# Performance work log

Hardware: AMD Instinct MI355X
Metric: run time of the kernel (lower is better)

The kernel has to match this reference:

```python
import jax, jax.numpy as jnp
import numpy as np

# hyperparameters (init_kwargs)
T = 0.1
MARGIN = 0.0
NEG_IOU = 0.5
K = 2              # pos_topk
WEIGHT = 1.0
EXPONENT = 2.0
NEG_SAMPLES = 512  # neg_samples_num
START_DNS_EPOCH = 1

# static problem sizes
B, SPB, TPS = 16, 2, 4          # videos, sentences/video, targets/sentence
N, C = 64, 256                  # clips, channels
S = B * SPB                     # total sentences = 32
M = S * TPS                     # total moments = 128


def setup_inputs() -> dict:
    key = jax.random.key(0)
    k1, k2, k3, k4 = jax.random.split(key, 4)
    return {
        "video_feats": jax.random.normal(k1, (S, C, N, N), jnp.float32),
        "sents_feats": jax.random.normal(k2, (S, C), jnp.float32),
        "num_sentences": jnp.full((B,), SPB, jnp.int32),
        "num_targets": jnp.full((S,), TPS, jnp.int32),
        "iou2d": jax.random.uniform(k3, (S, N, N), jnp.float32),
        "iou2ds": jax.random.uniform(k4, (M, N, N), jnp.float32),
        "mask2d": jnp.triu(jnp.ones((N, N), bool)),  # 2D-TAN valid-proposal mask
        "epoch": 2,
    }


def _normalize(x):
    return x / jnp.maximum(jnp.linalg.norm(x, axis=-1, keepdims=True), 1e-12)


def _loss_core(video_feats, sents_feats, iou2d, iou2ds,
               num_sentences, num_targets, mask2d, epoch):
    S_, C_, N_, _ = video_feats.shape
    B_ = num_sentences.shape[0]
    M_ = iou2ds.shape[0]
    P = N_ * (N_ + 1) // 2  # number of True in upper-triangular mask2d

    # masked_select(mask2d) -> gather flat proposal positions (static size P)
    flat_idx = jnp.nonzero(mask2d.reshape(-1), size=P)[0]
    vf = video_feats.reshape(S_, C_, N_ * N_)[:, :, flat_idx]        # (S,C,P)
    vf = _normalize(vf.transpose(0, 2, 1))                            # (S,P,C)
    _ = _normalize(sents_feats)                                       # normalized but unused downstream
    iou2d_f = iou2d.reshape(S_, -1)[:, flat_idx]                      # (S,P)
    iou2ds_f = iou2ds.reshape(M_, -1)[:, flat_idx]                    # (M,P)

    scatter_m2s = jnp.repeat(jnp.arange(S_), num_targets, total_repeat_length=M_)
    scatter_s2b = jnp.repeat(jnp.arange(B_), num_sentences, total_repeat_length=S_)
    scatter_b2s = jnp.concatenate([jnp.zeros((1,), jnp.int32),
                                   jnp.cumsum(num_sentences)[:-1].astype(jnp.int32)])

    # all (ref, pos) pairs within each sentence's num_targets*K topk slots (uniform -> static)
    nK = (M_ // S_) * K
    base = (jnp.arange(S_) * nK)[:, None, None]
    i = jnp.arange(nK)
    zero = jnp.zeros((nK,), jnp.int32)
    ref_idx = (base + i[None, :, None] + zero[None, None, :]).reshape(-1)   # (E,)
    pos_idx = (base + zero[None, :, None] + i[None, None, :]).reshape(-1)   # (E,)
    scatter_e2s = jnp.repeat(jnp.arange(S_), nK * nK)                        # (E,)

    # top-K proposals per moment by IoU
    topk_idx = jax.lax.top_k(iou2ds_f, K)[1]                                 # (M,K)
    allm = vf[scatter_m2s]                                                   # (M,P,C)
    topk_vf = jnp.take_along_axis(allm, topk_idx[:, :, None], axis=1)        # (M,K,C)
    pos_vf = topk_vf.reshape(M_ * K, C_)

    intra_pos = jnp.sum(pos_vf[ref_idx] * pos_vf[pos_idx], axis=-1)          # (E,)
    bank = vf[scatter_b2s].reshape(B_ * P, C_)                               # one sentence per video
    intra_all = pos_vf @ bank.T                                              # (M*K, B*P)

    # positive mask: own-video block, refined by iou2d > neg_iou
    own = scatter_s2b[:, None] == jnp.arange(B_)[None, :]                    # (S,B)
    s2v_pos = iou2d_f > NEG_IOU                                              # (S,P)
    pos_mask = jnp.where(own[:, :, None], s2v_pos[:, None, :], False).reshape(S_, B_ * P)

    if epoch >= START_DNS_EPOCH:
        # DNS: similarity-weighted negative sampling without replacement (Gumbel top-k)
        sim = (jnp.einsum('mkc,pc->mkp', topk_vf, bank).mean(axis=1) + 1.0) * 0.5   # (M,B*P)
        fused = jax.ops.segment_sum(sim, scatter_m2s, num_segments=S_)
        fused = fused / num_targets[:, None].astype(sim.dtype)                      # per-sentence mean
        fused = jnp.where(pos_mask, 0.0, fused ** EXPONENT)                          # (S,B*P)
        logw = jnp.where(fused > 0, jnp.log(jnp.maximum(fused, 1e-30)), -jnp.inf)
        u = jax.random.uniform(jax.random.key(42), fused.shape, minval=1e-7, maxval=1.0 - 1e-7)
        gumbel = -jnp.log(-jnp.log(u))
        samp_idx = jax.lax.top_k(logw + gumbel, NEG_SAMPLES)[1]                      # (S,NEG_SAMPLES)
        neg_mask = jnp.zeros((S_, B_ * P), jnp.float32).at[
            jnp.arange(S_)[:, None], samp_idx].set(1.0)
    else:
        neg_mask = (~pos_mask).astype(jnp.float32)

    # LogCrossEntropy (InfoNCE with explicit negative mask)
    all_e = intra_all[ref_idx]            # (E, B*P)
    neg_e = neg_mask[scatter_e2s]         # (E, B*P)
    pos_logit = (intra_pos - MARGIN) / T
    neg_sum = jnp.sum(jnp.exp(all_e / T) * neg_e, axis=-1)
    loss = jnp.mean(-(pos_logit - jnp.log(jnp.exp(pos_logit) + neg_sum)))
    return loss


def reference(video_feats, sents_feats, num_sentences, num_targets,
              iou2d, iou2ds, mask2d, epoch):
    loss = _loss_core(video_feats, sents_feats, iou2d, iou2ds,
                      num_sentences, num_targets, mask2d, epoch)
    return (loss * WEIGHT, loss)
```

## Files before the change

kernel.cpp:

```cpp
#include <hip/hip_runtime.h>
#include <math.h>
#include <stdint.h>

#define S_    32
#define BV_   16
#define M_    128
#define C_    256
#define NN    4096
#define P_    2080
#define BP    33280
#define NSAMP 512
#define EQCAP 2048

__device__ __forceinline__ uint32_t rotl32(uint32_t x, int n){ return (x<<n) | (x>>(32-n)); }

__device__ __forceinline__ void threefry2x32(uint32_t k0, uint32_t k1, uint32_t &x0, uint32_t &x1){
  uint32_t ks2 = k0 ^ k1 ^ 0x1BD11BDAu;
  x0 += k0; x1 += k1;
  #define TF_R(r) { x0 += x1; x1 = rotl32(x1, r); x1 ^= x0; }
  TF_R(13) TF_R(15) TF_R(26) TF_R(6)
  x0 += k1;  x1 += ks2 + 1u;
  TF_R(17) TF_R(29) TF_R(16) TF_R(24)
  x0 += ks2; x1 += k0 + 2u;
  TF_R(13) TF_R(15) TF_R(26) TF_R(6)
  x0 += k0;  x1 += k1 + 3u;
  TF_R(17) TF_R(29) TF_R(16) TF_R(24)
  x0 += k1;  x1 += ks2 + 4u;
  TF_R(13) TF_R(15) TF_R(26) TF_R(6)
  x0 += ks2; x1 += k0 + 5u;
  #undef TF_R
}

__global__ __launch_bounds__(256) void k_prep(const float* __restrict__ iou2ds,
                                              const float* __restrict__ vfeat,
                                              float* __restrict__ pos_vf,
                                              float* __restrict__ qsumT,
                                              int* __restrict__ counter){
  const int s = blockIdx.x;
  const int t = threadIdx.x;
  __shared__ float sv1[256], sv2[256];
  __shared__ int   si1[256], si2[256];
  __shared__ int   fpk_s[8];
  __shared__ float wsum[4];
  __shared__ float s_inv;

  if(s==0 && t==0) *counter = 0;

  for(int q=0; q<4; ++q){
    const float* row = iou2ds + (size_t)(s*4 + q)*NN;
    float v1=-1e30f, v2=-1e30f; int i1=0x7FFFFFFF, i2=0x7FFFFFFF;
    for(int f=t; f<NN; f+=256){
      int ti = f>>6, tj = f&63;
      if(tj < ti) continue;
      float v = row[f];
      if(v > v1 || (v == v1 && f < i1)){ v2=v1; i2=i1; v1=v; i1=f; }
      else if(v > v2 || (v == v2 && f < i2)){ v2=v; i2=f; }
    }
    sv1[t]=v1; sv2[t]=v2; si1[t]=i1; si2[t]=i2;
    for(int stp=128; stp>0; stp>>=1){
      __syncthreads();
      if(t < stp){
        float a1=sv1[t], a2=sv2[t]; int x1=si1[t], x2=si2[t];
        float b1=sv1[t+stp], b2=sv2[t+stp]; int y1=si1[t+stp], y2=si2[t+stp];
        float m1v, m2v; int m1i, m2i;
        bool aTop = (a1 > b1) || (a1 == b1 && x1 < y1);
        if(aTop){
          m1v=a1; m1i=x1;
          if((a2 > b1) || (a2 == b1 && x2 < y1)){ m2v=a2; m2i=x2; } else { m2v=b1; m2i=y1; }
        } else {
          m1v=b1; m1i=y1;
          if((b2 > a1) || (b2 == a1 && y2 < x1)){ m2v=b2; m2i=y2; } else { m2v=a1; m2i=x1; }
        }
        sv1[t]=m1v; sv2[t]=m2v; si1[t]=m1i; si2[t]=m2i;
      }
    }
    __syncthreads();
    if(t==0){ fpk_s[q*2+0]=si1[0]; fpk_s[q*2+1]=si2[0]; }
    __syncthreads();
  }

  float v[8];
  #pragma unroll
  for(int r=0;r<8;r++) v[r] = vfeat[((size_t)s*C_ + t)*NN + fpk_s[r]];

  float qs = 0.f;
  for(int r=0; r<8; ++r){
    float ss = v[r]*v[r];
    for(int o=32;o>0;o>>=1) ss += __shfl_down(ss, o, 64);
    if((t&63)==0) wsum[t>>6]=ss;
    __syncthreads();
    if(t==0){
      float tot = wsum[0]+wsum[1]+wsum[2]+wsum[3];
      s_inv = 1.0f / fmaxf(sqrtf(tot), 1e-12f);
    }
    __syncthreads();
    float pv = v[r] * s_inv;
    pos_vf[(size_t)(s*8+r)*C_ + t] = pv;
    qs += pv;
  }
  qsumT[t*32 + s] = qs;
}

__global__ __launch_bounds__(256) void k_bankkeys(const float* __restrict__ vfeat,
                                                  const float* __restrict__ qsumT,
                                                  const float* __restrict__ iou2d,
                                                  float* __restrict__ bank,
                                                  unsigned int* __restrict__ ukey){
  extern __shared__ char dyn_sm[];
  float* tile = (float*)dyn_sm;
  float* ssp  = (float*)dyn_sm + 256*65;
  float* invs = (float*)dyn_sm + 256*65 + 256;

  const int i = blockIdx.x;
  const int b = blockIdx.y;
  const int t = threadIdx.x;
  const int j = t & 63, cq = t >> 6;
  const float* basep = vfeat + (size_t)(2*b)*C_*NN + (size_t)i*64;

  float ssq = 0.f;
  for(int it=0; it<64; ++it){
    int cc = it*4 + cq;
    float v = basep[(size_t)cc*NN + j];
    tile[cc*65 + j] = v;
    ssq += v*v;
  }
  ssp[t] = ssq;
  __syncthreads();
  if(t < 64){
    float tot = ssp[t]+ssp[64+t]+ssp[128+t]+ssp[192+t];
    invs[t] = 1.0f/fmaxf(sqrtf(tot), 1e-12f);
  }
  __syncthreads();

  const int start = 64*i - (i*(i-1))/2;
  for(int jj=i; jj<64; ++jj){
    size_t row = (size_t)b*P_ + start + (jj - i);
    bank[row*C_ + t] = tile[t*65 + jj] * invs[jj];
  }

  const int lane = t & 63;
  const int sbase = __builtin_amdgcn_readfirstlane((t >> 6) * 8);
  float acc[8];
  #pragma unroll
  for(int k=0;k<8;k++) acc[k]=0.f;
  #pragma unroll 4
  for(int cc=0; cc<256; ++cc){
    float v = tile[cc*65 + lane];
    const float* qc = qsumT + cc*32 + sbase;
    #pragma unroll
    for(int k=0;k<8;k++) acc[k] = fmaf(qc[k], v, acc[k]);
  }

  if(lane >= i){
    const int jg = b*P_ + start + (lane - i);
    const int fp = i*64 + lane;
    const float iou0 = iou2d[(size_t)(2*b)*NN + fp];
    const float iou1 = iou2d[(size_t)(2*b+1)*NN + fp];
    const float inv_j = invs[lane];
    #pragma unroll 1
    for(int k=0;k<8;k++){
      const int sIdx = sbase + k;
      float fz = 0.0625f*(acc[k]*inv_j) + 0.5f;
      bool pos = ((sIdx>>1)==b) && (((sIdx&1)?iou1:iou0) > 0.5f);
      float val = pos ? 0.f : fz*fz;
      float key;
      if(val > 0.f){
        float logw = logf(fmaxf(val, 1e-30f));
        unsigned int f = (unsigned int)(sIdx*BP + jg);
        const unsigned int HALF = 532480u;
        bool second = f >= HALF;
        uint32_t x0 = second ? (f - HALF) : f;
        uint32_t x1 = second ? f : (f + HALF);
        threefry2x32(0u, 42u, x0, x1);
        uint32_t bits = second ? x1 : x0;
        uint32_t fb = (bits >> 9) | 0x3f800000u;
        float f01 = __uint_as_float(fb) - 1.0f;
        const float mn = 1e-7f, mx = 1.0f - 1e-7f;
        float u = fmaxf(mn, f01*(mx-mn) + mn);
        float g = -logf(-logf(u));
        key = logw + g;
      } else {
        key = -INFINITY;
      }
      unsigned int kb = __float_as_uint(key);
      kb = (kb & 0x80000000u) ? ~kb : (kb | 0x80000000u);
      ukey[(size_t)sIdx*BP + jg] = kb;
    }
  }
}

__global__ __launch_bounds__(1024) void k_selneg(const unsigned int* __restrict__ ukey,
                                                 const float* __restrict__ bank,
                                                 const float* __restrict__ pos_vf,
                                                 float* __restrict__ partial,
                                                 int* __restrict__ counter,
                                                 float* __restrict__ out){
  extern __shared__ char dyn_sm[];
  unsigned int* row  = (unsigned int*)dyn_sm;
  unsigned int* hist = (unsigned int*)dyn_sm + BP;
  int* list_lds = (int*)hist;
  int* eqbuf    = (int*)hist + 512;
  float* pv     = (float*)dyn_sm;
  float* hibuf  = (float*)dyn_sm + 4096;
  __shared__ int s_wv[16];
  __shared__ unsigned int s_prefix;
  __shared__ int s_cntgt, s_need, s_eq;
  __shared__ float red[8][8];
  __shared__ float ns_s[8];

  const int s = blockIdx.x;
  const int t = threadIdx.x;
  const int lane = t & 63;
  const int col  = t & 15;
  const unsigned int* grow = ukey + (size_t)s*BP;

  unsigned int prefix = 0, pmask = 0;
  int need = NSAMP, cnt_gt = 0;

  for(int lev=0; lev<4; ++lev){
    const int shift = 24 - 8*lev;
    for(int k=t; k<256*17; k+=1024) hist[k] = 0;
    __syncthreads();
    if(lev==0){
      for(int k=t; k<BP; k+=1024){
        unsigned int u = grow[k];
        row[k] = u;
        atomicAdd(&hist[(u >> 24)*17 + col], 1u);
      }
    } else {
      for(int k=t; k<BP; k+=1024){
        unsigned int u = row[k];
        if((u & pmask) == prefix)
          atomicAdd(&hist[((u >> shift) & 255u)*17 + col], 1u);
      }
    }
    __syncthreads();
    int v = 0; unsigned int h = 0;
    if(t < 256){
      const unsigned int* hr = hist + t*17;
      #pragma unroll
      for(int c=0;c<16;c++) h += hr[c];
      v = (int)h;
      #pragma unroll
      for(int off=1; off<64; off<<=1){
        int src = lane + off;
        int o = __shfl(v, (src<64)?src:lane, 64);
        v += (src<64)? o : 0;
      }
      if(lane==0) s_wv[t>>6] = v;
    }
    __syncthreads();
    if(t < 256){
      int wv4 = t>>6, tail = 0;
      for(int w2=wv4+1; w2<4; ++w2) tail += s_wv[w2];
      int Sb  = v + tail;
      int Sb1 = Sb - (int)h;
      if(Sb >= need && Sb1 < need){
        s_prefix = prefix | ((unsigned int)t << shift);
        s_cntgt  = cnt_gt + Sb1;
        s_need   = need - Sb1;
      }
    }
    __syncthreads();
    prefix = s_prefix; cnt_gt = s_cntgt; need = s_need;
    pmask |= (0xFFu << shift);
    __syncthreads();
  }

  const unsigned int ustar = prefix;
  const int quota = need;

  if(t==0) s_eq = 0;
  __syncthreads();

  int gtc = 0;
  for(int k=t; k<BP; k+=1024) gtc += (row[k] > ustar) ? 1 : 0;
  int vg = gtc;
  #pragma unroll
  for(int off=1; off<64; off<<=1){
    int src = lane - off;
    int o = __shfl(vg, (src>=0)?src:lane, 64);
    vg += (src>=0)? o : 0;
  }
  const int wv16 = t>>6;
  if(lane==63) s_wv[wv16] = vg;
  __syncthreads();
  int base2 = 0;
  for(int w2=0; w2<wv16; ++w2) base2 += s_wv[w2];
  int gi = base2 + vg - gtc;
  for(int k=t; k<BP; k+=1024){
    unsigned int u = row[k];
    if(u > ustar){
      list_lds[gi++] = k;
    } else if(u == ustar){
      int e = atomicAdd(&s_eq, 1);
      if(e < EQCAP) eqbuf[e] = k;
    }
  }
  __syncthreads();
  const int eqn = s_eq;
  if(eqn <= EQCAP){
    for(int i2=t; i2<eqn; i2+=1024){
      int ii = eqbuf[i2];
      int r = 0;
      for(int j2=0; j2<eqn; ++j2) r += (eqbuf[j2] < ii) ? 1 : 0;
      if(r < quota) list_lds[cnt_gt + r] = ii;
    }
  } else {
    if(t==0){
      int taken = 0;
      for(int idx=0; idx<BP && taken<quota; ++idx)
        if(row[idx]==ustar){ list_lds[cnt_gt + taken] = idx; ++taken; }
    }
  }
  __syncthreads();

  for(int idx=t; idx<8*C_; idx+=1024){
    int a = idx>>8, c = idx&255;
    pv[a*260 + c] = pos_vf[(size_t)(s*8)*C_ + idx];
  }
  __syncthreads();

  const int t0 = t & 511, half = t >> 9;
  const int jn = list_lds[t0];
  const float4* bp = (const float4*)(bank + (size_t)jn*C_ + half*128);
  float acc[8] = {0,0,0,0,0,0,0,0};
  for(int c4=0; c4<32; ++c4){
    float4 bv = bp[c4];
    #pragma unroll
    for(int a=0;a<8;a++){
      const float* pva = pv + a*260 + half*128 + c4*4;
      acc[a] += bv.x*pva[0] + bv.y*pva[1] + bv.z*pva[2] + bv.w*pva[3];
    }
  }
  if(half==1){
    #pragma unroll
    for(int a=0;a<8;a++) hibuf[t0*8 + a] = acc[a];
  }
  __syncthreads();
  if(t < 512){
    float e[8];
    #pragma unroll
    for(int a=0;a<8;a++){
      float accf = acc[a] + hibuf[t0*8 + a];
      float v = expf(accf/0.1f);
      for(int o=32;o>0;o>>=1) v += __shfl_down(v, o, 64);
      e[a] = v;
    }
    int wv = t>>6;
    if((t&63)==0){
      #pragma unroll
      for(int a=0;a<8;a++) red[wv][a]=e[a];
    }
  }
  __syncthreads();
  if(t < 8){
    float tot = 0.f;
    for(int w=0; w<8; w++) tot += red[w][t];
    ns_s[t] = tot;
  }
  __syncthreads();

  if(t < 64){
    int a = t>>3, b2 = t&7;
    float dot = 0.f;
    for(int c=0;c<C_;c++) dot += pv[a*260+c]*pv[b2*260+c];
    float pl = dot/0.1f;
    float term = logf(expf(pl) + ns_s[a]) - pl;
    for(int o=32;o>0;o>>=1) term += __shfl_down(term, o, 64);
    if(t==0){
      atomicExch(&partial[s], term);
      __threadfence();
      int old = atomicAdd(counter, 1);
      if(old == 31){
        __threadfence();
        float sum = 0.f;
        for(int i2=0;i2<32;i2++) sum += atomicAdd(&partial[i2], 0.0f);
        float loss = sum / 2048.0f;
        out[0] = loss * 1.0f;
        out[1] = loss;
      }
    }
  }
}

extern "C" void kernel_launch(void* const* d_in, const int* in_sizes, int n_in,
                              void* d_out, int out_size, void* d_ws, size_t ws_size,
                              hipStream_t stream) {
  const float* video_feats = (const float*)d_in[0];
  const float* iou2d  = (const float*)d_in[4];
  const float* iou2ds = (const float*)d_in[5];

  const size_t o_pvf   = 0;
  const size_t o_qsT   = 262144;
  const size_t o_bank  = 294912;
  const size_t o_ukey  = 34373632;
  const size_t o_part  = 38633472;
  const size_t o_cnt   = 38633600;
  const size_t NEED    = 38633728;
  if (ws_size < NEED) return;

  char* w = (char*)d_ws;
  float*        pos_vf  = (float*)(w + o_pvf);
  float*        qsumT   = (float*)(w + o_qsT);
  float*        bank    = (float*)(w + o_bank);
  unsigned int* ukey    = (unsigned int*)(w + o_ukey);
  float*        part    = (float*)(w + o_part);
  int*          counter = (int*)(w + o_cnt);
  float*        out     = (float*)d_out;

  const int BK_LDS  = (256*65 + 256 + 64) * 4;
  const int SEL_LDS = (BP + 256*17) * 4;
  static bool attr_set = false;
  if(!attr_set){
    (void)hipFuncSetAttribute((const void*)k_bankkeys,
                              hipFuncAttributeMaxDynamicSharedMemorySize, BK_LDS);
    (void)hipFuncSetAttribute((const void*)k_selneg,
                              hipFuncAttributeMaxDynamicSharedMemorySize, SEL_LDS);
    attr_set = true;
  }

  k_prep<<<32, 256, 0, stream>>>(iou2ds, video_feats, pos_vf, qsumT, counter);
  k_bankkeys<<<dim3(64,16), 256, BK_LDS, stream>>>(video_feats, qsumT, iou2d, bank, ukey);
  k_selneg<<<32, 1024, SEL_LDS, stream>>>(ukey, bank, pos_vf, part, counter, out);
}
```

Before: 165.2 us.

## Fuse first radix level into key kernel and split negative scoring into wide kernel

The key-generation kernel now also builds the top-byte histogram of the sort keys for each sentence, using LDS atomics that are flushed to a global histogram. This lets the selection kernel skip its first full radix pass. Selection reads keys straight from global memory instead of staging a 33K-entry row in LDS, which lowers LDS use and raises occupancy. The negative-similarity dot products move into a separate 256-block kernel with a last-block reduction, spreading the work that was previously confined to 32 blocks. The cost is an extra launch, global atomics, and repeated global reads of each key row during the remaining radix levels.

```diff
diff --git a/kernel.cpp b/kernel.cpp
--- a/kernel.cpp
+++ b/kernel.cpp
@@ -35,7 +35,8 @@
                                               const float* __restrict__ vfeat,
                                               float* __restrict__ pos_vf,
                                               float* __restrict__ qsumT,
-                                              int* __restrict__ counter){
+                                              unsigned int* __restrict__ ghist,
+                                              int* __restrict__ counters){
   const int s = blockIdx.x;
   const int t = threadIdx.x;
   __shared__ float sv1[256], sv2[256];
@@ -44,7 +45,8 @@
   __shared__ float wsum[4];
   __shared__ float s_inv;
 
-  if(s==0 && t==0) *counter = 0;
+  ghist[s*256 + t] = 0u;
+  if(s==0 && t==0){ counters[0]=0; counters[1]=0; }
 
   for(int q=0; q<4; ++q){
     const float* row = iou2ds + (size_t)(s*4 + q)*NN;
@@ -105,11 +107,13 @@
                                                   const float* __restrict__ qsumT,
                                                   const float* __restrict__ iou2d,
                                                   float* __restrict__ bank,
-                                                  unsigned int* __restrict__ ukey){
+                                                  unsigned int* __restrict__ ukey,
+                                                  unsigned int* __restrict__ ghist){
   extern __shared__ char dyn_sm[];
   float* tile = (float*)dyn_sm;
   float* ssp  = (float*)dyn_sm + 256*65;
   float* invs = (float*)dyn_sm + 256*65 + 256;
+  unsigned int* lh = (unsigned int*)dyn_sm;
 
   const int i = blockIdx.x;
   const int b = blockIdx.y;
@@ -150,6 +154,10 @@
     #pragma unroll
     for(int k=0;k<8;k++) acc[k] = fmaf(qc[k], v, acc[k]);
   }
+
+  __syncthreads();
+  for(int k=t; k<8192*2; k+=256) lh[k] = 0u;
+  __syncthreads();
 
   if(lane >= i){
     const int jg = b*P_ + start + (lane - i);
@@ -185,59 +193,77 @@
       unsigned int kb = __float_as_uint(key);
       kb = (kb & 0x80000000u) ? ~kb : (kb | 0x80000000u);
       ukey[(size_t)sIdx*BP + jg] = kb;
-    }
-  }
-}
-
-__global__ __launch_bounds__(1024) void k_selneg(const unsigned int* __restrict__ ukey,
-                                                 const float* __restrict__ bank,
-                                                 const float* __restrict__ pos_vf,
-                                                 float* __restrict__ partial,
-                                                 int* __restrict__ counter,
-                                                 float* __restrict__ out){
-  extern __shared__ char dyn_sm[];
-  unsigned int* row  = (unsigned int*)dyn_sm;
-  unsigned int* hist = (unsigned int*)dyn_sm + BP;
-  int* list_lds = (int*)hist;
-  int* eqbuf    = (int*)hist + 512;
-  float* pv     = (float*)dyn_sm;
-  float* hibuf  = (float*)dyn_sm + 4096;
+      atomicAdd(&lh[(sIdx*256 + (kb>>24))*2 + (lane&1)], 1u);
+    }
+  }
+  __syncthreads();
+  for(int bin=t; bin<8192; bin+=256){
+    unsigned int v = lh[bin*2] + lh[bin*2+1];
+    if(v) atomicAdd(&ghist[bin], v);
+  }
+}
+
+__global__ __launch_bounds__(1024) void k_select2(const unsigned int* __restrict__ ukey,
+                                                  const unsigned int* __restrict__ ghist,
+                                                  int* __restrict__ neglist){
+  __shared__ unsigned int hist2[256*17];
+  __shared__ int list_lds[NSAMP];
+  __shared__ int eqbuf[EQCAP];
   __shared__ int s_wv[16];
   __shared__ unsigned int s_prefix;
   __shared__ int s_cntgt, s_need, s_eq;
-  __shared__ float red[8][8];
-  __shared__ float ns_s[8];
 
   const int s = blockIdx.x;
   const int t = threadIdx.x;
   const int lane = t & 63;
-  const int col  = t & 15;
   const unsigned int* grow = ukey + (size_t)s*BP;
 
-  unsigned int prefix = 0, pmask = 0;
+  unsigned int prefix = 0, pmask = 0xFF000000u;
   int need = NSAMP, cnt_gt = 0;
 
-  for(int lev=0; lev<4; ++lev){
-    const int shift = 24 - 8*lev;
-    for(int k=t; k<256*17; k+=1024) hist[k] = 0;
-    __syncthreads();
-    if(lev==0){
-      for(int k=t; k<BP; k+=1024){
-        unsigned int u = grow[k];
-        row[k] = u;
-        atomicAdd(&hist[(u >> 24)*17 + col], 1u);
-      }
-    } else {
-      for(int k=t; k<BP; k+=1024){
-        unsigned int u = row[k];
-        if((u & pmask) == prefix)
-          atomicAdd(&hist[((u >> shift) & 255u)*17 + col], 1u);
-      }
-    }
-    __syncthreads();
+  {
     int v = 0; unsigned int h = 0;
     if(t < 256){
-      const unsigned int* hr = hist + t*17;
+      h = ghist[s*256 + t];
+      v = (int)h;
+      #pragma unroll
+      for(int off=1; off<64; off<<=1){
+        int src = lane + off;
+        int o = __shfl(v, (src<64)?src:lane, 64);
+        v += (src<64)? o : 0;
+      }
+      if(lane==0) s_wv[t>>6] = v;
+    }
+    __syncthreads();
+    if(t < 256){
+      int wv4 = t>>6, tail = 0;
+      for(int w2=wv4+1; w2<4; ++w2) tail += s_wv[w2];
+      int Sb  = v + tail;
+      int Sb1 = Sb - (int)h;
+      if(Sb >= need && Sb1 < need){
+        s_prefix = ((unsigned int)t) << 24;
+        s_cntgt  = Sb1;
+        s_need   = need - Sb1;
+      }
+    }
+    __syncthreads();
+    prefix = s_prefix; cnt_gt = s_cntgt; need = s_need;
+    __syncthreads();
+  }
+
+  for(int lev=0; lev<3; ++lev){
+    const int shift = 16 - 8*lev;
+    for(int k=t; k<256*17; k+=1024) hist2[k] = 0;
+    __syncthreads();
+    for(int k=t; k<BP; k+=1024){
+      unsigned int u = grow[k];
+      if((u & pmask) == prefix)
+        atomicAdd(&hist2[((u >> shift) & 255u)*17 + (t&15)], 1u);
+    }
+    __syncthreads();
+    int v = 0; unsigned int h = 0;
+    if(t < 256){
+      const unsigned int* hr = hist2 + t*17;
       #pragma unroll
       for(int c=0;c<16;c++) h += hr[c];
       v = (int)h;
@@ -256,7 +282,7 @@
       int Sb  = v + tail;
       int Sb1 = Sb - (int)h;
       if(Sb >= need && Sb1 < need){
-        s_prefix = prefix | ((unsigned int)t << shift);
+        s_prefix = prefix | (((unsigned int)t) << shift);
         s_cntgt  = cnt_gt + Sb1;
         s_need   = need - Sb1;
       }
@@ -274,7 +300,7 @@
   __syncthreads();
 
   int gtc = 0;
-  for(int k=t; k<BP; k+=1024) gtc += (row[k] > ustar) ? 1 : 0;
+  for(int k=t; k<BP; k+=1024) gtc += (grow[k] > ustar) ? 1 : 0;
   int vg = gtc;
   #pragma unroll
   for(int off=1; off<64; off<<=1){
@@ -289,7 +315,7 @@
   for(int w2=0; w2<wv16; ++w2) base2 += s_wv[w2];
   int gi = base2 + vg - gtc;
   for(int k=t; k<BP; k+=1024){
-    unsigned int u = row[k];
+    unsigned int u = grow[k];
     if(u > ustar){
       list_lds[gi++] = k;
     } else if(u == ustar){
@@ -310,76 +336,79 @@
     if(t==0){
       int taken = 0;
       for(int idx=0; idx<BP && taken<quota; ++idx)
-        if(row[idx]==ustar){ list_lds[cnt_gt + taken] = idx; ++taken; }
-    }
-  }
-  __syncthreads();
-
-  for(int idx=t; idx<8*C_; idx+=1024){
-    int a = idx>>8, c = idx&255;
-    pv[a*260 + c] = pos_vf[(size_t)(s*8)*C_ + idx];
-  }
-  __syncthreads();
-
-  const int t0 = t & 511, half = t >> 9;
-  const int jn = list_lds[t0];
-  const float4* bp = (const float4*)(bank + (size_t)jn*C_ + half*128);
-  float acc[8] = {0,0,0,0,0,0,0,0};
-  for(int c4=0; c4<32; ++c4){
-    float4 bv = bp[c4];
-    #pragma unroll
-    for(int a=0;a<8;a++){
-      const float* pva = pv + a*260 + half*128 + c4*4;
-      acc[a] += bv.x*pva[0] + bv.y*pva[1] + bv.z*pva[2] + bv.w*pva[3];
-    }
-  }
-  if(half==1){
-    #pragma unroll
-    for(int a=0;a<8;a++) hibuf[t0*8 + a] = acc[a];
-  }
-  __syncthreads();
-  if(t < 512){
-    float e[8];
-    #pragma unroll
-    for(int a=0;a<8;a++){
-      float accf = acc[a] + hibuf[t0*8 + a];
-      float v = expf(accf/0.1f);
-      for(int o=32;o>0;o>>=1) v += __shfl_down(v, o, 64);
-      e[a] = v;
-    }
-    int wv = t>>6;
-    if((t&63)==0){
-      #pragma unroll
-      for(int a=0;a<8;a++) red[wv][a]=e[a];
-    }
-  }
-  __syncthreads();
-  if(t < 8){
-    float tot = 0.f;
-    for(int w=0; w<8; w++) tot += red[w][t];
-    ns_s[t] = tot;
-  }
-  __syncthreads();
-
-  if(t < 64){
-    int a = t>>3, b2 = t&7;
-    float dot = 0.f;
-    for(int c=0;c<C_;c++) dot += pv[a*260+c]*pv[b2*260+c];
-    float pl = dot/0.1f;
-    float term = logf(expf(pl) + ns_s[a]) - pl;
-    for(int o=32;o>0;o>>=1) term += __shfl_down(term, o, 64);
+        if(grow[idx]==ustar){ list_lds[cnt_gt + taken] = idx; ++taken; }
+    }
+  }
+  __syncthreads();
+  if(t < NSAMP) neglist[s*NSAMP + t] = list_lds[t];
+}
+
+__global__ __launch_bounds__(512) void k_negfin(const float* __restrict__ bank,
+                                                const float* __restrict__ pos_vf,
+                                                const int* __restrict__ neglist,
+                                                float* __restrict__ ns_part,
+                                                int* __restrict__ counters,
+                                                float* __restrict__ out){
+  const int s   = blockIdx.x >> 3;
+  const int oct = blockIdx.x & 7;
+  const int t = threadIdx.x;
+  __shared__ float pv[8][C_];
+  __shared__ float terms[256];
+  __shared__ int s_last;
+
+  for(int idx=t; idx<8*C_; idx+=512) pv[idx>>8][idx&255] = pos_vf[(size_t)(s*8)*C_ + idx];
+  __syncthreads();
+
+  const int a = t >> 6;
+  const int n = t & 63;
+  const int j = neglist[s*NSAMP + oct*64 + n];
+  const float4* bp  = (const float4*)(bank + (size_t)j*C_);
+  const float4* pva = (const float4*)&pv[a][0];
+  float acc = 0.f;
+  #pragma unroll 8
+  for(int c4=0; c4<64; ++c4){
+    float4 bv = bp[c4], av = pva[c4];
+    acc += bv.x*av.x + bv.y*av.y + bv.z*av.z + bv.w*av.w;
+  }
+  float e = expf(acc/0.1f);
+  for(int o=32;o>0;o>>=1) e += __shfl_down(e, o, 64);
+  if(n==0) ns_part[((s*8 + a)*8) + oct] = e;
+
+  __threadfence();
+  __syncthreads();
+  if(t==0){
+    int old = atomicAdd(&counters[1], 1);
+    s_last = (old == 255) ? 1 : 0;
+  }
+  __syncthreads();
+
+  if(s_last){
+    __threadfence();
+    if(t < 256){
+      const int s2 = t>>3, a2 = t&7;
+      float ns = 0.f;
+      for(int oc=0; oc<8; ++oc) ns += atomicAdd(&ns_part[t*8 + oc], 0.0f);
+      const float4* A = (const float4*)(pos_vf + (size_t)(s2*8 + a2)*C_);
+      float termSum = 0.f;
+      for(int b2=0; b2<8; ++b2){
+        const float4* B = (const float4*)(pos_vf + (size_t)(s2*8 + b2)*C_);
+        float dot = 0.f;
+        for(int c4=0; c4<64; ++c4){
+          float4 av = A[c4], bv = B[c4];
+          dot += av.x*bv.x + av.y*bv.y + av.z*bv.z + av.w*bv.w;
+        }
+        float pl = dot/0.1f;
+        termSum += logf(expf(pl) + ns) - pl;
+      }
+      terms[t] = termSum;
+    }
+    __syncthreads();
     if(t==0){
-      atomicExch(&partial[s], term);
-      __threadfence();
-      int old = atomicAdd(counter, 1);
-      if(old == 31){
-        __threadfence();
-        float sum = 0.f;
-        for(int i2=0;i2<32;i2++) sum += atomicAdd(&partial[i2], 0.0f);
-        float loss = sum / 2048.0f;
-        out[0] = loss * 1.0f;
-        out[1] = loss;
-      }
+      float sum = 0.f;
+      for(int i2=0;i2<256;i2++) sum += terms[i2];
+      float loss = sum / 2048.0f;
+      out[0] = loss * 1.0f;
+      out[1] = loss;
     }
   }
 }
@@ -395,9 +424,11 @@
   const size_t o_qsT   = 262144;
   const size_t o_bank  = 294912;
   const size_t o_ukey  = 34373632;
-  const size_t o_part  = 38633472;
-  const size_t o_cnt   = 38633600;
-  const size_t NEED    = 38633728;
+  const size_t o_gh    = 38633472;
+  const size_t o_list  = 38666240;
+  const size_t o_nsp   = 38731776;
+  const size_t o_cnt   = 38739968;
+  const size_t NEED    = 38740224;
   if (ws_size < NEED) return;
 
   char* w = (char*)d_ws;
@@ -405,22 +436,22 @@
   float*        qsumT   = (float*)(w + o_qsT);
   float*        bank    = (float*)(w + o_bank);
   unsigned int* ukey    = (unsigned int*)(w + o_ukey);
-  float*        part    = (float*)(w + o_part);
-  int*          counter = (int*)(w + o_cnt);
+  unsigned int* ghist   = (unsigned int*)(w + o_gh);
+  int*          neglist = (int*)(w + o_list);
+  float*        ns_part = (float*)(w + o_nsp);
+  int*          counters= (int*)(w + o_cnt);
   float*        out     = (float*)d_out;
 
-  const int BK_LDS  = (256*65 + 256 + 64) * 4;
-  const int SEL_LDS = (BP + 256*17) * 4;
+  const int BK_LDS = (256*65 + 256 + 64) * 4;
   static bool attr_set = false;
   if(!attr_set){
     (void)hipFuncSetAttribute((const void*)k_bankkeys,
                               hipFuncAttributeMaxDynamicSharedMemorySize, BK_LDS);
-    (void)hipFuncSetAttribute((const void*)k_selneg,
-                              hipFuncAttributeMaxDynamicSharedMemorySize, SEL_LDS);
     attr_set = true;
   }
 
-  k_prep<<<32, 256, 0, stream>>>(iou2ds, video_feats, pos_vf, qsumT, counter);
-  k_bankkeys<<<dim3(64,16), 256, BK_LDS, stream>>>(video_feats, qsumT, iou2d, bank, ukey);
-  k_selneg<<<32, 1024, SEL_LDS, stream>>>(ukey, bank, pos_vf, part, counter, out);
-}
+  k_prep<<<32, 256, 0, stream>>>(iou2ds, video_feats, pos_vf, qsumT, ghist, counters);
+  k_bankkeys<<<dim3(64,16), 256, BK_LDS, stream>>>(video_feats, qsumT, iou2d, bank, ukey, ghist);
+  k_select2<<<32, 1024, 0, stream>>>(ukey, ghist, neglist);
+  k_negfin<<<256, 512, 0, stream>>>(bank, pos_vf, neglist, ns_part, counters, out);
+}
```

Measured after the change: 274.1 us. +65.9%, slower.
